# Kernel optimization log

Hardware: AMD Instinct MI355X
Metric: run time of the kernel (lower is better)

## Reference

```python
import jax, jax.numpy as jnp
import numpy as np

B, C, N = 2, 512, 2048
HEADS, DIM_HEAD, SCALE = 16, 64, 8.0
H_DIM = HEADS * DIM_HEAD
EPS = 1e-12  # F.normalize default eps


def setup_inputs() -> dict:
    key = jax.random.key(0)
    ks = jax.random.split(key, 5)
    x = jax.random.normal(ks[0], (B, C, N), dtype=jnp.float32)
    Wqkv = jax.random.normal(ks[1], (3 * H_DIM, C), dtype=jnp.float32) * (1.0 / np.sqrt(C))
    q_scale = jnp.ones((DIM_HEAD,), dtype=jnp.float32)
    k_scale = jnp.ones((DIM_HEAD,), dtype=jnp.float32)
    Wout = jax.random.normal(ks[2], (C, H_DIM), dtype=jnp.float32) * (1.0 / np.sqrt(H_DIM))
    bout = jax.random.normal(ks[3], (C,), dtype=jnp.float32) * 0.01
    return {"x": x, "Wqkv": Wqkv, "q_scale": q_scale, "k_scale": k_scale,
            "Wout": Wout, "bout": bout}


def _l2norm(t):
    # F.normalize(t, dim=-1): t / max(||t||, eps)
    n = jnp.sqrt(jnp.sum(t * t, axis=-1, keepdims=True))
    return t / jnp.maximum(n, EPS)


def reference(x, Wqkv, q_scale, k_scale, Wout, bout):
    # 1x1 conv == pointwise matmul over channel dim
    qkv = jnp.einsum('oc,bcn->bon', Wqkv, x)              # [B, 3*H_DIM, N]
    q, k, v = jnp.split(qkv, 3, axis=1)
    # unflatten channels -> [B, H, D, N]
    def to_heads(t):
        return t.reshape(B, HEADS, DIM_HEAD, N)
    q, k, v = map(to_heads, (q, k, v))
    # cosine attention: l2-normalize q,k over head dim, apply learned per-dim scales
    q = _l2norm(q.transpose(0, 1, 3, 2)) * q_scale        # [B, H, N, D]
    k = _l2norm(k.transpose(0, 1, 3, 2)) * k_scale        # [B, H, N, D]
    sim = jnp.einsum('bhid,bhjd->bhij', q, k) * SCALE     # [B, H, N, N]
    attn = jax.nn.softmax(sim, axis=-1)
    out = jnp.einsum('bhij,bhdj->bhid', attn, v)          # [B, H, N, D]
    out = out.transpose(0, 1, 3, 2).reshape(B, H_DIM, N)  # b h n d -> b (h d) n
    return jnp.einsum('oc,bcn->bon', Wout, out) + bout[None, :, None]
```

## Files before the change

kernel.cpp:

```cpp
#include <hip/hip_runtime.h>
#include <hip/hip_bf16.h>

#define BATCH 2
#define CCH   512
#define NSEQ  2048
#define HEADS 16
#define DHEAD 64
#define HDIM  1024
#define ODIM  3072
#define QK_PRESCALE 11.541560327111707f

typedef short short4v __attribute__((ext_vector_type(4)));
typedef short short8 __attribute__((ext_vector_type(8)));
typedef float float4v __attribute__((ext_vector_type(4)));
typedef int   int4v   __attribute__((ext_vector_type(4)));

__device__ __forceinline__ unsigned short f2bf(float f) {
    unsigned int u = __float_as_uint(f);
    return (unsigned short)((u + 0x7FFFu + ((u >> 16) & 1u)) >> 16);
}
__device__ __forceinline__ unsigned short f2bf_fast(float f) {
    return (unsigned short)((__float_as_uint(f) + 0x8000u) >> 16);
}
__device__ __forceinline__ float fexp2(float x) {
#if __has_builtin(__builtin_amdgcn_exp2f)
    return __builtin_amdgcn_exp2f(x);
#else
    return exp2f(x);
#endif
}
__device__ __forceinline__ int pack_bf16(float lo, float hi) {
#if __has_builtin(__builtin_amdgcn_cvt_pk_bf16_f32)
    typedef __bf16 bf2_t __attribute__((ext_vector_type(2)));
    bf2_t v = __builtin_amdgcn_cvt_pk_bf16_f32(lo, hi);
    return __builtin_bit_cast(int, v);
#else
    return (int)f2bf_fast(lo) | ((int)(unsigned)f2bf_fast(hi) << 16);
#endif
}

typedef __attribute__((address_space(1))) const void* as1_cvp;
typedef __attribute__((address_space(3))) void* as3_vp;
__device__ __forceinline__ void cp16(const void* g, void* l) {
    __builtin_amdgcn_global_load_lds((as1_cvp)g, (as3_vp)l, 16, 0, 0);
}
__global__ __launch_bounds__(256) void k_prep(
    const float* __restrict__ Wqkv, const float* __restrict__ Wout,
    const float* __restrict__ x,
    const float* __restrict__ qs, const float* __restrict__ ks,
    unsigned short* __restrict__ Wqkvb, unsigned short* __restrict__ Woutb,
    unsigned short* __restrict__ xt, float* __restrict__ M) {
    const int bx = blockIdx.x;
    if (bx < 2048) {
        if (bx == 0 && threadIdx.x < 64) {
            int lane = threadIdx.x;
            float p = fabsf(qs[lane] * ks[lane]);
#pragma unroll
            for (int off = 1; off < 64; off <<= 1) p = fmaxf(p, __shfl_xor(p, off));
            if (lane == 0) *M = QK_PRESCALE * p;
        }
        int i4 = (bx * 256 + threadIdx.x) * 4;
        const float* src; unsigned short* dst; int idx;
        if (i4 < ODIM * CCH) { src = Wqkv; dst = Wqkvb; idx = i4; }
        else { src = Wout; dst = Woutb; idx = i4 - ODIM * CCH; }
        float4 v = *(const float4*)(src + idx);
        ushort4 o;
        o.x = f2bf(v.x); o.y = f2bf(v.y); o.z = f2bf(v.z); o.w = f2bf(v.w);
        *(ushort4*)(dst + idx) = o;
        return;
    }
    __shared__ unsigned short t[64][65];
    const int fx = bx - 2048;
    const int n0 = (fx & 31) * 64;
    const int c0 = ((fx >> 5) & 7) * 64;
    const int b  = fx >> 8;
    const int tr = threadIdx.x >> 6, tc = threadIdx.x & 63;
    const float* xs = x + (size_t)b * CCH * NSEQ;
    unsigned short* xd = xt + (size_t)b * NSEQ * CCH;
#pragma unroll
    for (int r = 0; r < 16; ++r) {
        int c = r * 4 + tr;
        t[c][tc] = f2bf(xs[(size_t)(c0 + c) * NSEQ + n0 + tc]);
    }
    __syncthreads();
#pragma unroll
    for (int r = 0; r < 16; ++r) {
        int n = r * 4 + tr;
        xd[(size_t)(n0 + n) * CCH + c0 + tc] = t[tc][n];
    }
}

__global__ __launch_bounds__(256) void k_gemm_qkv(
    const unsigned short* __restrict__ W, const unsigned short* __restrict__ xt,
    const float* __restrict__ qs, const float* __restrict__ ks,
    unsigned short* __restrict__ qh, unsigned short* __restrict__ kh,
    unsigned short* __restrict__ vb) {
    constexpr int K = CCH, N = NSEQ;
    __shared__ __align__(16) short smem[2 * 128 * 64];
    short* lsA = smem;
    short* lsB = smem + 128 * 64;
    const int tid = threadIdx.x, wave = tid >> 6, lane = tid & 63;
    const int l15 = lane & 15, quad = lane >> 4;
    const int n0 = blockIdx.x * 128, m0 = blockIdx.y * 128, z = blockIdx.z;
    const short* Ab = (const short*)W + (size_t)m0 * K;
    const short* Bb = (const short*)xt + ((size_t)z * N + n0) * K;
    const int wm = wave >> 1, wn = wave & 1;
    const int cswz = (((tid & 7) ^ ((tid >> 3) & 7))) * 8;
    const int sw7 = (l15 & 7);

    float4v acc[4][4];
#pragma unroll
    for (int i = 0; i < 4; ++i)
#pragma unroll
        for (int j = 0; j < 4; ++j) acc[i][j] = (float4v){0.f, 0.f, 0.f, 0.f};

    for (int k0 = 0; k0 < K; k0 += 64) {
#pragma unroll
        for (int it = 0; it < 4; ++it) {
            int row = it * 32 + (tid >> 3);
            cp16(Ab + (size_t)row * K + k0 + cswz, &lsA[it * 2048 + wave * 512]);
            cp16(Bb + (size_t)row * K + k0 + cswz, &lsB[it * 2048 + wave * 512]);
        }
        __syncthreads();
        short8 af[4][2], bfr[4][2];
#pragma unroll
        for (int t = 0; t < 4; ++t)
#pragma unroll
            for (int kk = 0; kk < 2; ++kk) {
                af[t][kk]  = *(const short8*)&lsA[(wm * 64 + t * 16 + l15) * 64 + ((kk * 4 + quad) ^ sw7) * 8];
                bfr[t][kk] = *(const short8*)&lsB[(wn * 64 + t * 16 + l15) * 64 + ((kk * 4 + quad) ^ sw7) * 8];
            }
#pragma unroll
        for (int mt = 0; mt < 4; ++mt)
#pragma unroll
            for (int nt = 0; nt < 4; ++nt) {
                acc[mt][nt] = __builtin_amdgcn_mfma_f32_16x16x32_bf16(af[mt][0], bfr[nt][0], acc[mt][nt], 0, 0, 0);
                acc[mt][nt] = __builtin_amdgcn_mfma_f32_16x16x32_bf16(af[mt][1], bfr[nt][1], acc[mt][nt], 0, 0, 0);
            }
        __syncthreads();
    }

    const int co   = (m0 + wm * 64) >> 6;
    const int part = co >> 4;
    const int h    = co & 15;
    const int bh   = z * HEADS + h;
    short* myT = smem + wave * 4096;

    if (part < 2) {
        float inv[4];
#pragma unroll
        for (int nt = 0; nt < 4; ++nt) {
            float ss = 0.f;
#pragma unroll
            for (int mt = 0; mt < 4; ++mt)
#pragma unroll
                for (int r = 0; r < 4; ++r) ss += acc[mt][nt][r] * acc[mt][nt][r];
            ss += __shfl_xor(ss, 16);
            ss += __shfl_xor(ss, 32);
            inv[nt] = 1.0f / fmaxf(sqrtf(ss), 1e-12f);
        }
        const float* sc = part ? ks : qs;
        const float csc = part ? 1.0f : QK_PRESCALE;
#pragma unroll
        for (int mt = 0; mt < 4; ++mt) {
            const int db = mt * 16 + quad * 4;
            float4 s4 = *(const float4*)(sc + db);
            s4.x *= csc; s4.y *= csc; s4.z *= csc; s4.w *= csc;
#pragma unroll
            for (int nt = 0; nt < 4; ++nt) {
                int nl = nt * 16 + l15;
                short4v o;
                o.x = (short)f2bf(acc[mt][nt][0] * inv[nt] * s4.x);
                o.y = (short)f2bf(acc[mt][nt][1] * inv[nt] * s4.y);
                o.z = (short)f2bf(acc[mt][nt][2] * inv[nt] * s4.z);
                o.w = (short)f2bf(acc[mt][nt][3] * inv[nt] * s4.w);
                *(short4v*)&myT[nl * 64 + (((db >> 3) ^ (nl & 7)) << 3) + (db & 7)] = o;
            }
        }
        unsigned short* dst = (part ? kh : qh) + (size_t)bh * NSEQ * DHEAD
                              + (size_t)(n0 + wn * 64) * DHEAD;
#pragma unroll
        for (int pass = 0; pass < 8; ++pass) {
            int nl = pass * 8 + (lane >> 3), c = lane & 7;
            short8 vv = *(const short8*)&myT[nl * 64 + ((c ^ (nl & 7)) << 3)];
            *(short8*)&dst[(size_t)nl * DHEAD + c * 8] = vv;
        }
    } else {
#pragma unroll
        for (int mt = 0; mt < 4; ++mt)
#pragma unroll
            for (int nt = 0; nt < 4; ++nt) {
                int nl = nt * 16 + l15;
                int swc = nl >> 3, swo = nl & 7;
#pragma unroll
                for (int r = 0; r < 4; ++r) {
                    int d = mt * 16 + quad * 4 + r;
                    myT[d * 64 + ((swc ^ (d & 7)) << 3) + swo] = (short)f2bf(acc[mt][nt][r]);
                }
            }
        unsigned short* dst = vb + (size_t)bh * DHEAD * NSEQ + n0 + wn * 64;
#pragma unroll
        for (int pass = 0; pass < 8; ++pass) {
            int d = pass * 8 + (lane >> 3), c = lane & 7;
            short8 vv = *(const short8*)&myT[d * 64 + ((c ^ (d & 7)) << 3)];
            *(short8*)&dst[(size_t)d * NSEQ + c * 8] = vv;
        }
    }
}

#define KVB 32
__global__ __launch_bounds__(512, 4) void k_attn(
    const unsigned short* __restrict__ qh, const unsigned short* __restrict__ kh,
    const unsigned short* __restrict__ vb,
    unsigned short* __restrict__ aot, const float* __restrict__ Mptr) {
    __shared__ __align__(16) short Kt[2][4][KVB * 64];
    __shared__ __align__(16) short Vt[2][4][64 * KVB];
    const int tid = threadIdx.x, wave = tid >> 6, lane = tid & 63;
    const int grp = wave >> 2, w4 = wave & 3;
    const int gtid = tid & 255;
    const int l15 = lane & 15, quad = lane >> 4, q8 = quad * 8;
    const int flat = blockIdx.x;
    const int xcd = flat & 7, idx = flat >> 3;
    const int bh = xcd * 4 + (idx >> 4);
    const int i0 = (idx & 15) * 128;
    const int b = bh >> 4, h = bh & 15;
    const float Ms = *Mptr;
    const float4v mInit = (float4v){-Ms, -Ms, -Ms, -Ms};
    const int srowK = gtid >> 3;
    const int kkey  = (srowK & 3) | (((srowK >> 3) & 1) << 2);
    const int cswzK = ((gtid & 7) ^ kkey) * 8;
    const int srowV = gtid >> 2;
    const int cswzV = ((gtid & 3) ^ ((srowV >> 1) & 3)) * 8;
    const int ksw = l15 & 7;
    const int kc0 = ((0 + quad) ^ ksw) * 8;
    const int kc1 = ((4 + quad) ^ ksw) * 8;
    const int vkr = (l15 >> 1) & 3;
    const int ar0 = (l15 >> 2) * 8 + (l15 & 3);
    const int ar1 = ar0 + 4;
    const int jbase = grp * (NSEQ / 2);

    short8 qf[2][2];
    {
        const short* qb = (const short*)qh + ((size_t)bh * NSEQ + i0 + w4 * 32) * DHEAD;
#pragma unroll
        for (int it = 0; it < 2; ++it) {
            qf[it][0] = *(const short8*)&qb[(it * 16 + l15) * DHEAD + q8];
            qf[it][1] = *(const short8*)&qb[(it * 16 + l15) * DHEAD + 32 + q8];
        }
    }

    float4v of[2][4];
#pragma unroll
    for (int it = 0; it < 2; ++it)
#pragma unroll
        for (int dt = 0; dt < 4; ++dt) of[it][dt] = (float4v){0.f, 0.f, 0.f, 0.f};
    float l_acc[2] = {0.f, 0.f};

    const short* kbase = (const short*)kh + ((size_t)bh * NSEQ + jbase) * DHEAD;
    const short* vbase = (const short*)vb + (size_t)bh * DHEAD * NSEQ + jbase;

    short8 pb0c, pb1c, avc[4];

#define STAGE(T_, B_) do {                                                       \
        cp16(kbase + (size_t)((T_) * KVB + srowK) * DHEAD + cswzK,               \
             &Kt[grp][B_][w4 * 512]);                                            \
        cp16(vbase + (size_t)srowV * NSEQ + (T_) * KVB + cswzV,                  \
             &Vt[grp][B_][w4 * 512]);                                            \
    } while (0)

#define STEP(CB_, DO_PV_) do {                                                   \
        const short* Kb = &Kt[grp][CB_][0];                                      \
        const short* Vb = &Vt[grp][CB_][0];                                      \
        __builtin_amdgcn_s_setprio(1);                                           \
        short8 k00 = *(const short8*)&Kb[ar0 * 64 + kc0];                        \
        short8 k01 = *(const short8*)&Kb[ar0 * 64 + kc1];                        \
        short8 k10 = *(const short8*)&Kb[ar1 * 64 + kc0];                        \
        short8 k11 = *(const short8*)&Kb[ar1 * 64 + kc1];                        \
        float4v s00 = __builtin_amdgcn_mfma_f32_16x16x32_bf16(k00, qf[0][0], mInit, 0, 0, 0); \
        float4v s01 = __builtin_amdgcn_mfma_f32_16x16x32_bf16(k00, qf[1][0], mInit, 0, 0, 0); \
        float4v s10 = __builtin_amdgcn_mfma_f32_16x16x32_bf16(k10, qf[0][0], mInit, 0, 0, 0); \
        float4v s11 = __builtin_amdgcn_mfma_f32_16x16x32_bf16(k10, qf[1][0], mInit, 0, 0, 0); \
        s00 = __builtin_amdgcn_mfma_f32_16x16x32_bf16(k01, qf[0][1], s00, 0, 0, 0); \
        s01 = __builtin_amdgcn_mfma_f32_16x16x32_bf16(k01, qf[1][1], s01, 0, 0, 0); \
        s10 = __builtin_amdgcn_mfma_f32_16x16x32_bf16(k11, qf[0][1], s10, 0, 0, 0); \
        s11 = __builtin_amdgcn_mfma_f32_16x16x32_bf16(k11, qf[1][1], s11, 0, 0, 0); \
        if (DO_PV_) {                                                            \
            _Pragma("unroll")                                                    \
            for (int dt = 0; dt < 4; ++dt) {                                     \
                of[0][dt] = __builtin_amdgcn_mfma_f32_16x16x32_bf16(avc[dt], pb0c, of[0][dt], 0, 0, 0); \
                of[1][dt] = __builtin_amdgcn_mfma_f32_16x16x32_bf16(avc[dt], pb1c, of[1][dt], 0, 0, 0); \
            }                                                                    \
        }                                                                        \
        int4v pw0, pw1;                                                          \
        {                                                                        \
            float p0, p1, p2, p3;                                                \
            p0 = fexp2(s00[0]); p1 = fexp2(s00[1]); p2 = fexp2(s00[2]); p3 = fexp2(s00[3]); \
            l_acc[0] += (p0 + p1) + (p2 + p3);                                   \
            pw0[0] = pack_bf16(p0, p1); pw0[1] = pack_bf16(p2, p3);              \
            p0 = fexp2(s10[0]); p1 = fexp2(s10[1]); p2 = fexp2(s10[2]); p3 = fexp2(s10[3]); \
            l_acc[0] += (p0 + p1) + (p2 + p3);                                   \
            pw0[2] = pack_bf16(p0, p1); pw0[3] = pack_bf16(p2, p3);              \
            p0 = fexp2(s01[0]); p1 = fexp2(s01[1]); p2 = fexp2(s01[2]); p3 = fexp2(s01[3]); \
            l_acc[1] += (p0 + p1) + (p2 + p3);                                   \
            pw1[0] = pack_bf16(p0, p1); pw1[1] = pack_bf16(p2, p3);              \
            p0 = fexp2(s11[0]); p1 = fexp2(s11[1]); p2 = fexp2(s11[2]); p3 = fexp2(s11[3]); \
            l_acc[1] += (p0 + p1) + (p2 + p3);                                   \
            pw1[2] = pack_bf16(p0, p1); pw1[3] = pack_bf16(p2, p3);              \
        }                                                                        \
        pb0c = __builtin_bit_cast(short8, pw0);                                  \
        pb1c = __builtin_bit_cast(short8, pw1);                                  \
        _Pragma("unroll")                                                        \
        for (int dt = 0; dt < 4; ++dt)                                           \
            avc[dt] = *(const short8*)&Vb[(dt * 16 + l15) * KVB + ((quad ^ vkr) * 8)]; \
        __builtin_amdgcn_s_setprio(0);                                           \
    } while (0)

#define WAITBAR(N_) do {                                                         \
        asm volatile("s_waitcnt vmcnt(" #N_ ")" ::: "memory");                   \
        __builtin_amdgcn_s_barrier();                                            \
        __builtin_amdgcn_sched_barrier(0);                                       \
    } while (0)

    constexpr int T = (NSEQ / 2) / KVB;
    STAGE(0, 0);
    STAGE(1, 1);
    STAGE(2, 2);
    WAITBAR(4);
    STEP(0, 0);
#pragma unroll 4
    for (int t = 1; t <= T - 3; ++t) {
        STAGE(t + 2, (t + 2) & 3);
        WAITBAR(4);
        STEP(t & 3, 1);
    }
    WAITBAR(2);
    STEP((T - 2) & 3, 1);
    WAITBAR(0);
    STEP((T - 1) & 3, 1);
#pragma unroll
    for (int dt = 0; dt < 4; ++dt) {
        of[0][dt] = __builtin_amdgcn_mfma_f32_16x16x32_bf16(avc[dt], pb0c, of[0][dt], 0, 0, 0);
        of[1][dt] = __builtin_amdgcn_mfma_f32_16x16x32_bf16(avc[dt], pb1c, of[1][dt], 0, 0, 0);
    }
#undef STAGE
#undef STEP
#undef WAITBAR

    float lred[2];
#pragma unroll
    for (int it = 0; it < 2; ++it) {
        float l = l_acc[it];
        l += __shfl_xor(l, 16);
        l += __shfl_xor(l, 32);
        lred[it] = l;
    }

    __syncthreads();

    float* F = (float*)&Kt[0][0][0];
    float* L = (float*)&Vt[0][0][0];
    if (grp == 1) {
#pragma unroll
        for (int it = 0; it < 2; ++it) {
#pragma unroll
            for (int dt = 0; dt < 4; ++dt)
                *(float4v*)&F[(((w4 * 2 + it) * 4 + dt) * 64 + lane) * 4] = of[it][dt];
            L[(w4 * 2 + it) * 64 + lane] = lred[it];
        }
    }
    __syncthreads();
    if (grp == 0) {
#pragma unroll
        for (int it = 0; it < 2; ++it) {
            float lt = lred[it] + L[(w4 * 2 + it) * 64 + lane];
            float inv = 1.0f / fmaxf(lt, 1e-30f);
            unsigned short* ob = aot + ((size_t)b * NSEQ + i0 + w4 * 32 + it * 16 + l15) * HDIM + h * DHEAD;
#pragma unroll
            for (int dt = 0; dt < 4; ++dt) {
                float4v p = *(const float4v*)&F[(((w4 * 2 + it) * 4 + dt) * 64 + lane) * 4];
                ushort4 o;
                o.x = f2bf((of[it][dt][0] + p[0]) * inv);
                o.y = f2bf((of[it][dt][1] + p[1]) * inv);
                o.z = f2bf((of[it][dt][2] + p[2]) * inv);
                o.w = f2bf((of[it][dt][3] + p[3]) * inv);
                *(ushort4*)&ob[dt * 16 + quad * 4] = o;
            }
        }
    }
}

__global__ __launch_bounds__(256) void k_gemm_out(
    const unsigned short* __restrict__ W, const unsigned short* __restrict__ aot,
    const float* __restrict__ bias, float* __restrict__ out) {
    constexpr int K = HDIM, N = NSEQ, M = CCH;
    __shared__ __align__(16) short lsA[64 * 64];
    __shared__ __align__(16) short lsB[64 * 64];
    const int tid = threadIdx.x, wave = tid >> 6, lane = tid & 63;
    const int l15 = lane & 15, quad = lane >> 4;
    const int n0 = blockIdx.x * 64, m0 = blockIdx.y * 64, z = blockIdx.z;
    const short* Ab = (const short*)W + (size_t)m0 * K;
    const short* Bb = (const short*)aot + ((size_t)z * N + n0) * K;
    const int wm = wave >> 1, wn = wave & 1;
    const int cswz = (((tid & 7) ^ ((tid >> 3) & 7))) * 8;
    const int sw7 = (l15 & 7);

    float4v acc[2][2];
#pragma unroll
    for (int i = 0; i < 2; ++i)
#pragma unroll
        for (int j = 0; j < 2; ++j) acc[i][j] = (float4v){0.f, 0.f, 0.f, 0.f};

    for (int k0 = 0; k0 < K; k0 += 64) {
        {
            int row = tid >> 3;
            cp16(Ab + (size_t)row * K + k0 + cswz, &lsA[wave * 512]);
            cp16(Ab + (size_t)(row + 32) * K + k0 + cswz, &lsA[2048 + wave * 512]);
            cp16(Bb + (size_t)row * K + k0 + cswz, &lsB[wave * 512]);
            cp16(Bb + (size_t)(row + 32) * K + k0 + cswz, &lsB[2048 + wave * 512]);
        }
        __syncthreads();
        short8 af[2][2], bfr[2][2];
#pragma unroll
        for (int t = 0; t < 2; ++t)
#pragma unroll
            for (int kk = 0; kk < 2; ++kk) {
                af[t][kk]  = *(const short8*)&lsA[(wm * 32 + t * 16 + l15) * 64 + ((kk * 4 + quad) ^ sw7) * 8];
                bfr[t][kk] = *(const short8*)&lsB[(wn * 32 + t * 16 + l15) * 64 + ((kk * 4 + quad) ^ sw7) * 8];
            }
#pragma unroll
        for (int mt = 0; mt < 2; ++mt)
#pragma unroll
            for (int nt = 0; nt < 2; ++nt) {
                acc[mt][nt] = __builtin_amdgcn_mfma_f32_16x16x32_bf16(af[mt][0], bfr[nt][0], acc[mt][nt], 0, 0, 0);
                acc[mt][nt] = __builtin_amdgcn_mfma_f32_16x16x32_bf16(af[mt][1], bfr[nt][1], acc[mt][nt], 0, 0, 0);
            }
        __syncthreads();
    }
    float* Co = out + (size_t)z * M * N;
#pragma unroll
    for (int mt = 0; mt < 2; ++mt)
#pragma unroll
        for (int nt = 0; nt < 2; ++nt) {
            int mrow = m0 + wm * 32 + mt * 16 + quad * 4;
#pragma unroll
            for (int r = 0; r < 4; ++r) {
                int mr = mrow + r;
                int nc = n0 + wn * 32 + nt * 16 + l15;
                Co[(size_t)mr * N + nc] = acc[mt][nt][r] + bias[mr];
            }
        }
}

extern "C" void kernel_launch(void* const* d_in, const int* in_sizes, int n_in,
                              void* d_out, int out_size, void* d_ws, size_t ws_size,
                              hipStream_t stream) {
    const float* x = nullptr; const float* Wqkv = nullptr;
    const float* qs = nullptr; const float* ks = nullptr;
    const float* Wout = nullptr; const float* bout = nullptr;
    for (int i = 0; i < n_in; ++i) {
        switch (in_sizes[i]) {
            case BATCH * CCH * NSEQ: x    = (const float*)d_in[i]; break;
            case ODIM * CCH:         Wqkv = (const float*)d_in[i]; break;
            case CCH * HDIM:         Wout = (const float*)d_in[i]; break;
            case CCH:                bout = (const float*)d_in[i]; break;
            case DHEAD: if (!qs) qs = (const float*)d_in[i]; else ks = (const float*)d_in[i]; break;
            default: break;
        }
    }
    float* y = (float*)d_out;

    char* ws = (char*)d_ws;
    float*          Mbuf  = (float*)(ws + 0);
    unsigned short* Wqkvb = (unsigned short*)(ws + 4096);
    unsigned short* Woutb = (unsigned short*)(ws + 3149824);
    unsigned short* xt    = (unsigned short*)(ws + 4198400);
    unsigned short* qh    = (unsigned short*)(ws + 8392704);
    unsigned short* kh    = (unsigned short*)(ws + 16781312);
    unsigned short* vb    = (unsigned short*)(ws + 25169920);
    unsigned short* aot   = (unsigned short*)(ws + 33558528);

    k_prep<<<dim3(2048 + 512), 256, 0, stream>>>(Wqkv, Wout, x, qs, ks, Wqkvb, Woutb, xt, Mbuf);
    k_gemm_qkv<<<dim3(NSEQ / 128, ODIM / 128, BATCH), 256, 0, stream>>>(Wqkvb, xt, qs, ks, qh, kh, vb);
    k_attn<<<dim3(512), 512, 0, stream>>>(qh, kh, vb, aot, Mbuf);
    k_gemm_out<<<dim3(NSEQ / 64, CCH / 64, BATCH), 256, 0, stream>>>(Woutb, aot, bout, y);
}
```

Before: 142.9 us.

## Split attention waves into QK/softmax producers and PV consumers via LDS

Replaces the split-KV scheme, where two wave groups each handled half the keys and merged partial outputs at the end, with warp specialization. Four producer waves compute QK^T and exp over the full sequence and write bf16 probabilities to a double-buffered LDS tile. Four consumer waves load V and run the PV MFMAs one step behind. This removes the final partial-output merge and balances MFMA against exp work across waves. In exchange it adds an LDS round trip for P, a barrier every step, and a pipeline where each wave type may stall on the other.

```diff
diff --git a/kernel.cpp b/kernel.cpp
--- a/kernel.cpp
+++ b/kernel.cpp
@@ -213,11 +213,13 @@
     const unsigned short* __restrict__ qh, const unsigned short* __restrict__ kh,
     const unsigned short* __restrict__ vb,
     unsigned short* __restrict__ aot, const float* __restrict__ Mptr) {
-    __shared__ __align__(16) short Kt[2][4][KVB * 64];
-    __shared__ __align__(16) short Vt[2][4][64 * KVB];
+    __shared__ __align__(16) short Kt[4][KVB * 64];
+    __shared__ __align__(16) short Vt[4][64 * KVB];
+    __shared__ __align__(16) short Pt[2][4][32 * 32];
+    __shared__ float Ls[4][2][64];
     const int tid = threadIdx.x, wave = tid >> 6, lane = tid & 63;
-    const int grp = wave >> 2, w4 = wave & 3;
-    const int gtid = tid & 255;
+    const bool prod = wave < 4;
+    const int w4 = wave & 3;
     const int l15 = lane & 15, quad = lane >> 4, q8 = quad * 8;
     const int flat = blockIdx.x;
     const int xcd = flat & 7, idx = flat >> 3;
@@ -226,21 +228,31 @@
     const int b = bh >> 4, h = bh & 15;
     const float Ms = *Mptr;
     const float4v mInit = (float4v){-Ms, -Ms, -Ms, -Ms};
-    const int srowK = gtid >> 3;
+    const int srowK = w4 * 8 + (lane >> 3);
     const int kkey  = (srowK & 3) | (((srowK >> 3) & 1) << 2);
-    const int cswzK = ((gtid & 7) ^ kkey) * 8;
-    const int srowV = gtid >> 2;
-    const int cswzV = ((gtid & 3) ^ ((srowV >> 1) & 3)) * 8;
+    const int cswzK = ((lane & 7) ^ kkey) * 8;
+    const int srowV = w4 * 16 + (lane >> 2);
+    const int cswzV = ((lane & 3) ^ ((srowV >> 1) & 3)) * 8;
     const int ksw = l15 & 7;
     const int kc0 = ((0 + quad) ^ ksw) * 8;
     const int kc1 = ((4 + quad) ^ ksw) * 8;
     const int vkr = (l15 >> 1) & 3;
+    const int pswz = ((quad ^ (l15 & 3)) * 8);
     const int ar0 = (l15 >> 2) * 8 + (l15 & 3);
     const int ar1 = ar0 + 4;
-    const int jbase = grp * (NSEQ / 2);
+
+    const short* kbase = (const short*)kh + (size_t)bh * NSEQ * DHEAD;
+    const short* vbase = (const short*)vb + (size_t)bh * DHEAD * NSEQ;
 
     short8 qf[2][2];
-    {
+    float l_acc[2] = {0.f, 0.f};
+    float4v of[2][4];
+#pragma unroll
+    for (int it = 0; it < 2; ++it)
+#pragma unroll
+        for (int dt = 0; dt < 4; ++dt) of[it][dt] = (float4v){0.f, 0.f, 0.f, 0.f};
+
+    if (prod) {
         const short* qb = (const short*)qh + ((size_t)bh * NSEQ + i0 + w4 * 32) * DHEAD;
 #pragma unroll
         for (int it = 0; it < 2; ++it) {
@@ -249,28 +261,13 @@
         }
     }
 
-    float4v of[2][4];
-#pragma unroll
-    for (int it = 0; it < 2; ++it)
-#pragma unroll
-        for (int dt = 0; dt < 4; ++dt) of[it][dt] = (float4v){0.f, 0.f, 0.f, 0.f};
-    float l_acc[2] = {0.f, 0.f};
-
-    const short* kbase = (const short*)kh + ((size_t)bh * NSEQ + jbase) * DHEAD;
-    const short* vbase = (const short*)vb + (size_t)bh * DHEAD * NSEQ + jbase;
-
-    short8 pb0c, pb1c, avc[4];
-
-#define STAGE(T_, B_) do {                                                       \
-        cp16(kbase + (size_t)((T_) * KVB + srowK) * DHEAD + cswzK,               \
-             &Kt[grp][B_][w4 * 512]);                                            \
-        cp16(vbase + (size_t)srowV * NSEQ + (T_) * KVB + cswzV,                  \
-             &Vt[grp][B_][w4 * 512]);                                            \
-    } while (0)
-
-#define STEP(CB_, DO_PV_) do {                                                   \
-        const short* Kb = &Kt[grp][CB_][0];                                      \
-        const short* Vb = &Vt[grp][CB_][0];                                      \
+#define STAGE_K(T_, B_) \
+    cp16(kbase + (size_t)((T_) * KVB + srowK) * DHEAD + cswzK, &Kt[B_][w4 * 512])
+#define STAGE_V(T_, B_) \
+    cp16(vbase + (size_t)srowV * NSEQ + (T_) * KVB + cswzV, &Vt[B_][w4 * 512])
+
+#define PRODUCE(T_) do {                                                         \
+        const short* Kb = &Kt[(T_) & 3][0];                                      \
         __builtin_amdgcn_s_setprio(1);                                           \
         short8 k00 = *(const short8*)&Kb[ar0 * 64 + kc0];                        \
         short8 k01 = *(const short8*)&Kb[ar0 * 64 + kc1];                        \
@@ -284,13 +281,6 @@
         s01 = __builtin_amdgcn_mfma_f32_16x16x32_bf16(k01, qf[1][1], s01, 0, 0, 0); \
         s10 = __builtin_amdgcn_mfma_f32_16x16x32_bf16(k11, qf[0][1], s10, 0, 0, 0); \
         s11 = __builtin_amdgcn_mfma_f32_16x16x32_bf16(k11, qf[1][1], s11, 0, 0, 0); \
-        if (DO_PV_) {                                                            \
-            _Pragma("unroll")                                                    \
-            for (int dt = 0; dt < 4; ++dt) {                                     \
-                of[0][dt] = __builtin_amdgcn_mfma_f32_16x16x32_bf16(avc[dt], pb0c, of[0][dt], 0, 0, 0); \
-                of[1][dt] = __builtin_amdgcn_mfma_f32_16x16x32_bf16(avc[dt], pb1c, of[1][dt], 0, 0, 0); \
-            }                                                                    \
-        }                                                                        \
         int4v pw0, pw1;                                                          \
         {                                                                        \
             float p0, p1, p2, p3;                                                \
@@ -307,86 +297,82 @@
             l_acc[1] += (p0 + p1) + (p2 + p3);                                   \
             pw1[2] = pack_bf16(p0, p1); pw1[3] = pack_bf16(p2, p3);              \
         }                                                                        \
-        pb0c = __builtin_bit_cast(short8, pw0);                                  \
-        pb1c = __builtin_bit_cast(short8, pw1);                                  \
-        _Pragma("unroll")                                                        \
-        for (int dt = 0; dt < 4; ++dt)                                           \
-            avc[dt] = *(const short8*)&Vb[(dt * 16 + l15) * KVB + ((quad ^ vkr) * 8)]; \
+        short* Pb = &Pt[(T_) & 1][w4][0];                                        \
+        *(short8*)&Pb[(0 * 16 + l15) * 32 + pswz] = __builtin_bit_cast(short8, pw0); \
+        *(short8*)&Pb[(1 * 16 + l15) * 32 + pswz] = __builtin_bit_cast(short8, pw1); \
         __builtin_amdgcn_s_setprio(0);                                           \
     } while (0)
 
-#define WAITBAR(N_) do {                                                         \
-        asm volatile("s_waitcnt vmcnt(" #N_ ")" ::: "memory");                   \
-        __builtin_amdgcn_s_barrier();                                            \
-        __builtin_amdgcn_sched_barrier(0);                                       \
+#define CONSUME(U_) do {                                                         \
+        const short* Vb = &Vt[(U_) & 3][0];                                      \
+        const short* Pb = &Pt[(U_) & 1][w4][0];                                  \
+        short8 av0 = *(const short8*)&Vb[(0 * 16 + l15) * KVB + ((quad ^ vkr) * 8)]; \
+        short8 av1 = *(const short8*)&Vb[(1 * 16 + l15) * KVB + ((quad ^ vkr) * 8)]; \
+        short8 av2 = *(const short8*)&Vb[(2 * 16 + l15) * KVB + ((quad ^ vkr) * 8)]; \
+        short8 av3 = *(const short8*)&Vb[(3 * 16 + l15) * KVB + ((quad ^ vkr) * 8)]; \
+        short8 pb0 = *(const short8*)&Pb[(0 * 16 + l15) * 32 + pswz];            \
+        short8 pb1 = *(const short8*)&Pb[(1 * 16 + l15) * 32 + pswz];            \
+        of[0][0] = __builtin_amdgcn_mfma_f32_16x16x32_bf16(av0, pb0, of[0][0], 0, 0, 0); \
+        of[1][0] = __builtin_amdgcn_mfma_f32_16x16x32_bf16(av0, pb1, of[1][0], 0, 0, 0); \
+        of[0][1] = __builtin_amdgcn_mfma_f32_16x16x32_bf16(av1, pb0, of[0][1], 0, 0, 0); \
+        of[1][1] = __builtin_amdgcn_mfma_f32_16x16x32_bf16(av1, pb1, of[1][1], 0, 0, 0); \
+        of[0][2] = __builtin_amdgcn_mfma_f32_16x16x32_bf16(av2, pb0, of[0][2], 0, 0, 0); \
+        of[1][2] = __builtin_amdgcn_mfma_f32_16x16x32_bf16(av2, pb1, of[1][2], 0, 0, 0); \
+        of[0][3] = __builtin_amdgcn_mfma_f32_16x16x32_bf16(av3, pb0, of[0][3], 0, 0, 0); \
+        of[1][3] = __builtin_amdgcn_mfma_f32_16x16x32_bf16(av3, pb1, of[1][3], 0, 0, 0); \
     } while (0)
 
-    constexpr int T = (NSEQ / 2) / KVB;
-    STAGE(0, 0);
-    STAGE(1, 1);
-    STAGE(2, 2);
-    WAITBAR(4);
-    STEP(0, 0);
-#pragma unroll 4
-    for (int t = 1; t <= T - 3; ++t) {
-        STAGE(t + 2, (t + 2) & 3);
-        WAITBAR(4);
-        STEP(t & 3, 1);
-    }
-    WAITBAR(2);
-    STEP((T - 2) & 3, 1);
-    WAITBAR(0);
-    STEP((T - 1) & 3, 1);
-#pragma unroll
-    for (int dt = 0; dt < 4; ++dt) {
-        of[0][dt] = __builtin_amdgcn_mfma_f32_16x16x32_bf16(avc[dt], pb0c, of[0][dt], 0, 0, 0);
-        of[1][dt] = __builtin_amdgcn_mfma_f32_16x16x32_bf16(avc[dt], pb1c, of[1][dt], 0, 0, 0);
-    }
-#undef STAGE
-#undef STEP
-#undef WAITBAR
+    constexpr int T = NSEQ / KVB;
+    if (prod) { STAGE_K(0, 0); STAGE_K(1, 1); }
+    else      { STAGE_V(0, 0); }
+
+    for (int t = 0; t < T; ++t) {
+        if (prod) STAGE_K((t + 2) & (T - 1), (t + 2) & 3);
+        else      STAGE_V((t + 1) & (T - 1), (t + 1) & 3);
+        asm volatile("s_waitcnt vmcnt(2)" ::: "memory");
+        asm volatile("s_waitcnt lgkmcnt(0)" ::: "memory");
+        __builtin_amdgcn_s_barrier();
+        __builtin_amdgcn_sched_barrier(0);
+        if (prod) PRODUCE(t);
+        else if (t) CONSUME(t - 1);
+    }
 
     float lred[2];
-#pragma unroll
-    for (int it = 0; it < 2; ++it) {
-        float l = l_acc[it];
-        l += __shfl_xor(l, 16);
-        l += __shfl_xor(l, 32);
-        lred[it] = l;
-    }
-
-    __syncthreads();
-
-    float* F = (float*)&Kt[0][0][0];
-    float* L = (float*)&Vt[0][0][0];
-    if (grp == 1) {
+    if (prod) {
 #pragma unroll
         for (int it = 0; it < 2; ++it) {
-#pragma unroll
-            for (int dt = 0; dt < 4; ++dt)
-                *(float4v*)&F[(((w4 * 2 + it) * 4 + dt) * 64 + lane) * 4] = of[it][dt];
-            L[(w4 * 2 + it) * 64 + lane] = lred[it];
-        }
-    }
-    __syncthreads();
-    if (grp == 0) {
+            float l = l_acc[it];
+            l += __shfl_xor(l, 16);
+            l += __shfl_xor(l, 32);
+            Ls[w4][it][lane] = l;
+        }
+    }
+    asm volatile("s_waitcnt lgkmcnt(0)" ::: "memory");
+    __builtin_amdgcn_s_barrier();
+    __builtin_amdgcn_sched_barrier(0);
+    if (!prod) {
+        asm volatile("s_waitcnt vmcnt(0)" ::: "memory");
+        CONSUME(T - 1);
 #pragma unroll
         for (int it = 0; it < 2; ++it) {
-            float lt = lred[it] + L[(w4 * 2 + it) * 64 + lane];
+            float lt = Ls[w4][it][lane];
             float inv = 1.0f / fmaxf(lt, 1e-30f);
             unsigned short* ob = aot + ((size_t)b * NSEQ + i0 + w4 * 32 + it * 16 + l15) * HDIM + h * DHEAD;
 #pragma unroll
             for (int dt = 0; dt < 4; ++dt) {
-                float4v p = *(const float4v*)&F[(((w4 * 2 + it) * 4 + dt) * 64 + lane) * 4];
                 ushort4 o;
-                o.x = f2bf((of[it][dt][0] + p[0]) * inv);
-                o.y = f2bf((of[it][dt][1] + p[1]) * inv);
-                o.z = f2bf((of[it][dt][2] + p[2]) * inv);
-                o.w = f2bf((of[it][dt][3] + p[3]) * inv);
+                o.x = f2bf(of[it][dt][0] * inv);
+                o.y = f2bf(of[it][dt][1] * inv);
+                o.z = f2bf(of[it][dt][2] * inv);
+                o.w = f2bf(of[it][dt][3] * inv);
                 *(ushort4*)&ob[dt * 16 + quad * 4] = o;
             }
         }
     }
+#undef STAGE_K
+#undef STAGE_V
+#undef PRODUCE
+#undef CONSUME
 }
 
 __global__ __launch_bounds__(256) void k_gemm_out(
```

Result: slower. 155.9 us (+9.1%).
